# Kernel optimization log

Measured on AMD Instinct MI355X. Metric: run time of the kernel, lower is better.

Reference implementation:

```python
import jax, jax.numpy as jnp
import numpy as np

B, NA, NR, D, H, DH = 2, 4096, 512, 128, 8, 16
N_LOCAL, N_IPA, N_ITER = 5, 4, 3


def rots_from_vec(v):
    # quaternion (1, vx, vy, vz) normalized -> rotation matrix (AlphaFold-style update)
    q = jnp.concatenate([jnp.ones(v.shape[:-1] + (1,), v.dtype), v], axis=-1)
    q = q / jnp.linalg.norm(q, axis=-1, keepdims=True)
    w, x, y, z = q[..., 0], q[..., 1], q[..., 2], q[..., 3]
    R = jnp.stack([
        1 - 2 * (y * y + z * z), 2 * (x * y - w * z), 2 * (x * z + w * y),
        2 * (x * y + w * z), 1 - 2 * (x * x + z * z), 2 * (y * z - w * x),
        2 * (x * z - w * y), 2 * (y * z + w * x), 1 - 2 * (x * x + y * y)], axis=-1)
    return R.reshape(v.shape[:-1] + (3, 3))


def apply_frames(R, t, x):
    return jnp.einsum('...ij,...j->...i', R, x) + t


def invert_frames(R, t):
    Rt = jnp.swapaxes(R, -1, -2)
    return Rt, -jnp.einsum('...ij,...j->...i', Rt, t)


def pool_atoms_to_res(atom_feats, res_map):
    # scatter-mean: atoms -> residues
    d = atom_feats.shape[-1]
    idx = (res_map + jnp.arange(B, dtype=res_map.dtype)[:, None] * NR).reshape(-1)
    sums = jax.ops.segment_sum(atom_feats.reshape(-1, d), idx, num_segments=B * NR)
    cnts = jax.ops.segment_sum(jnp.ones((B * NA, 1), atom_feats.dtype), idx, num_segments=B * NR)
    return (sums / (cnts + 1e-8)).reshape(B, NR, d)


def setup_inputs() -> dict:
    key = jax.random.key(0)
    ks = iter(jax.random.split(key, 40))
    s = 0.02
    inp = dict(
        coords_bad=jax.random.normal(next(ks), (B, NA, 3), jnp.float32) * 5.0,
        atom_types=jax.random.randint(next(ks), (B, NA), 0, 20),
        residue_types=jax.random.randint(next(ks), (B, NA), 0, 21),
        mask=jnp.ones((B, NA), jnp.float32),
        res_mask=jnp.ones((B, NR), jnp.float32),
        res_map=jnp.sort(jax.random.randint(next(ks), (B, NA), 0, NR), axis=-1),
        rots_bad=rots_from_vec(0.1 * jax.random.normal(next(ks), (B, NR, 3), jnp.float32)),
        trans_bad=jax.random.normal(next(ks), (B, NR, 3), jnp.float32) * 5.0,
        atom_emb=jax.random.normal(next(ks), (20, D), jnp.float32) * s,
        res_emb=jax.random.normal(next(ks), (21, D), jnp.float32) * s,
        coord_W=jax.random.normal(next(ks), (3, D), jnp.float32) * s,
        coord_b=jnp.zeros((D,), jnp.float32),
        local_W=jax.random.normal(next(ks), (N_LOCAL, D, D), jnp.float32) * s,
        local_b=jnp.zeros((N_LOCAL, D), jnp.float32),
        pair_W=jax.random.normal(next(ks), (4, D), jnp.float32) * s,
        pair_b=jnp.zeros((D,), jnp.float32),
        ipa_Wq=jax.random.normal(next(ks), (N_IPA, D, H * DH), jnp.float32) * s,
        ipa_Wk=jax.random.normal(next(ks), (N_IPA, D, H * DH), jnp.float32) * s,
        ipa_Wv=jax.random.normal(next(ks), (N_IPA, D, H * DH), jnp.float32) * s,
        ipa_Wb=jax.random.normal(next(ks), (N_IPA, D, H), jnp.float32) * s,
        ipa_Wo=jax.random.normal(next(ks), (N_IPA, H * DH, D), jnp.float32) * s,
        ipa_bo=jnp.zeros((N_IPA, D), jnp.float32),
        head_W=jax.random.normal(next(ks), (D, 6), jnp.float32) * s,
        head_b=jnp.zeros((6,), jnp.float32),
    )
    return inp


def reference(coords_bad, atom_types, residue_types, mask, res_mask, res_map,
              rots_bad, trans_bad, atom_emb, res_emb, coord_W, coord_b,
              local_W, local_b, pair_W, pair_b,
              ipa_Wq, ipa_Wk, ipa_Wv, ipa_Wb, ipa_Wo, ipa_bo, head_W, head_b):
    cur_R, cur_t = rots_bad, trans_bad
    mask_j = (res_mask > 0)[:, None, None, :]  # [B,1,1,NR]
    # encoder output is iteration-invariant (coords_bad fixed), hoist it
    atom_feats = atom_emb[atom_types] + res_emb[residue_types] + coords_bad @ coord_W + coord_b
    feats0 = pool_atoms_to_res(atom_feats, res_map)  # [B,NR,D]
    for _ in range(N_ITER):
        feats = feats0
        residual = feats
        for l in range(N_LOCAL):
            feats = jax.nn.gelu(feats @ local_W[l] + local_b[l]) + residual
            residual = feats
        rel = cur_t[:, :, None, :] - cur_t[:, None, :, :]          # [B,NR,NR,3]
        dist = jnp.linalg.norm(rel, axis=-1, keepdims=True)
        pairwise = jnp.concatenate([rel, dist], axis=-1) @ pair_W + pair_b  # [B,NR,NR,D]
        for l in range(N_IPA):
            q = (feats @ ipa_Wq[l]).reshape(B, NR, H, DH)
            k = (feats @ ipa_Wk[l]).reshape(B, NR, H, DH)
            v = (feats @ ipa_Wv[l]).reshape(B, NR, H, DH)
            bias = jnp.transpose(pairwise @ ipa_Wb[l], (0, 3, 1, 2))  # [B,H,NR,NR]
            logits = jnp.einsum('bihd,bjhd->bhij', q, k) / np.float32(np.sqrt(DH)) + bias
            logits = jnp.where(mask_j, logits, jnp.float32(-1e9))
            attn = jax.nn.softmax(logits, axis=-1)
            o = jnp.einsum('bhij,bjhd->bihd', attn, v).reshape(B, NR, H * DH)
            feats = (o @ ipa_Wo[l] + ipa_bo[l]) + residual
            residual = feats
        upd = feats @ head_W + head_b                      # [B,NR,6]
        rot_vec, trans_vec = upd[..., :3], upd[..., 3:]
        cur_R = jnp.einsum('...ij,...jk->...ik', rots_from_vec(rot_vec), cur_R)
        cur_t = cur_t + jnp.einsum('...ij,...j->...i', cur_R, trans_vec)
        cur_t = cur_t * res_mask[..., None]
    inv_R, inv_t = invert_frames(rots_bad, trans_bad)
    bidx = jnp.arange(B)[:, None]
    local = apply_frames(inv_R[bidx, res_map], inv_t[bidx, res_map], coords_bad)
    final = apply_frames(jnp.swapaxes(cur_R[bidx, res_map], -1, -2), cur_t[bidx, res_map], local)
    return cur_R, cur_t, final
```

## Files before the change

kernel.cpp:

```cpp
#include <hip/hip_runtime.h>
#include <math.h>

#define B_ 2
#define NA_ 4096
#define NR_ 512
#define D_ 128
#define H_ 8
#define DH_ 16
#define NLOCAL_ 5
#define NIPA_ 4
#define NITER_ 3

typedef _Float16 half2_t __attribute__((ext_vector_type(2)));
typedef _Float16 f16x4 __attribute__((ext_vector_type(4)));
typedef float f32x4 __attribute__((ext_vector_type(4)));

#if __has_builtin(__builtin_amdgcn_fdot2)
#define FDOT2(a, b, c) __builtin_amdgcn_fdot2((a), (b), (c), false)
#else
__device__ __forceinline__ float FDOT2(half2_t a, half2_t b, float c) {
  return c + (float)a.x * (float)b.x + (float)a.y * (float)b.y;
}
#endif

#define MFMA16(a, b, c) __builtin_amdgcn_mfma_f32_16x16x16f16((a), (b), (c), 0, 0, 0)

__device__ __forceinline__ unsigned int pack_h(float a, float b) {
  union { unsigned int u; half2_t h; } x;
  x.h = half2_t{(_Float16)a, (_Float16)b};
  return x.u;
}
__device__ __forceinline__ half2_t u2h(unsigned int u) {
  union { unsigned int u; half2_t h; } x;
  x.u = u;
  return x.h;
}
__device__ __forceinline__ f16x4 mk4(unsigned int a, unsigned int b) {
  union { uint2 u; f16x4 h; } x;
  x.u = make_uint2(a, b);
  return x.h;
}
__device__ __forceinline__ float gelu_tanh(float x) {
  float x3 = x * x * x;
  return 0.5f * x * (1.0f + tanhf(0.7978845608028654f * (x + 0.044715f * x3)));
}

__device__ __forceinline__ void store_vT(unsigned int* vw, int h, int u, int rr,
                                         float b0, float b1) {
  unsigned int pk = pack_h(b0, b1);
  unsigned short* vt16 = (unsigned short*)vw;
  vt16[((h * 16 + 2 * u) << 10) + rr] = (unsigned short)(pk & 0xffffu);
  vt16[((h * 16 + 2 * u + 1) << 10) + rr] = (unsigned short)(pk >> 16);
}

__global__ __launch_bounds__(256) void k_setup(
    const float* __restrict__ coords, const int* __restrict__ atype,
    const int* __restrict__ rtype, const int* __restrict__ res_map,
    const float* __restrict__ rots_bad, const float* __restrict__ trans_bad,
    const float* __restrict__ res_mask,
    const float* __restrict__ atom_emb, const float* __restrict__ res_emb,
    const float* __restrict__ coord_W, const float* __restrict__ coord_b,
    const float* __restrict__ local_W, const float* __restrict__ pair_W,
    const float* __restrict__ pair_b, const float* __restrict__ Wq,
    const float* __restrict__ Wk, const float* __restrict__ Wv, const float* __restrict__ Wb,
    const float* __restrict__ Wo, float* __restrict__ feats0, float* __restrict__ weff,
    float* __restrict__ beff, float* __restrict__ curR, float* __restrict__ curT0,
    float4* __restrict__ ts4g0, unsigned int* __restrict__ lwh,
    unsigned int* __restrict__ qkvh, unsigned int* __restrict__ woh) {
  int tid = threadIdx.x, bid = blockIdx.x;
  int gtid = (bid << 8) + tid;
  for (int t = gtid; t < 172032; t += 65536) {
    if (t < 40960) {
      int c = t & 127, kk = (t >> 7) & 63, l = t >> 13;
      const float* s = local_W + (size_t)l * 16384 + (2 * kk) * 128 + c;
      lwh[t] = pack_h(s[0], s[128]);
    } else if (t < 139264) {
      int t2 = t - 40960;
      int c = t2 & 127, kk = (t2 >> 7) & 63, lm = t2 >> 13;
      int l = lm / 3, m = lm % 3;
      const float* base = (m == 0) ? Wq : ((m == 1) ? Wk : Wv);
      const float* s = base + (size_t)l * 16384 + (2 * kk) * 128 + c;
      qkvh[t2] = pack_h(s[0], s[128]);
    } else {
      int t3 = t - 139264;
      int c = t3 & 127, kk = (t3 >> 7) & 63, l = t3 >> 13;
      const float* s = Wo + (size_t)l * 16384 + (2 * kk) * 128 + c;
      woh[t3] = pack_h(s[0], s[128]);
    }
  }
  if (gtid < 160) {
    int l = gtid / 40, rest = gtid % 40;
    int c = rest / 8, h = rest & 7;
    const float* row = (c < 4) ? (pair_W + c * D_) : pair_b;
    float acc = 0.f;
    for (int d = 0; d < D_; d++) acc += row[d] * Wb[l * D_ * H_ + d * H_ + h];
    if (c < 4) weff[l * 32 + c * 8 + h] = acc;
    else beff[l * 8 + h] = acc;
  }
  if (gtid < 9216) curR[gtid] = rots_bad[gtid];
  else if (gtid < 12288) curT0[gtid - 9216] = trans_bad[gtid - 9216];
  if (gtid < 1024)
    ts4g0[gtid] = make_float4(trans_bad[gtid * 3], trans_bad[gtid * 3 + 1],
                              trans_bad[gtid * 3 + 2], res_mask[gtid]);
  for (int rp = 0; rp < 2; rp++) {
    int row = (bid << 2) + (rp << 1) + (tid >> 7);
    int d = tid & 127;
    int b = row >> 9, rr = row & (NR_ - 1);
    const int* rm = res_map + b * NA_;
    int lo = 0, hi = NA_;
    while (lo < hi) { int mid = (lo + hi) >> 1; if (rm[mid] < rr) lo = mid + 1; else hi = mid; }
    int start = lo;
    hi = NA_;
    while (lo < hi) { int mid = (lo + hi) >> 1; if (rm[mid] < rr + 1) lo = mid + 1; else hi = mid; }
    int end = lo;
    float w0 = coord_W[d], w1 = coord_W[D_ + d], w2 = coord_W[2 * D_ + d], cb = coord_b[d];
    float s = 0.f;
    for (int a = start; a < end; a++) {
      int ga = b * NA_ + a;
      s += atom_emb[atype[ga] * D_ + d] + res_emb[rtype[ga] * D_ + d] +
           coords[ga * 3 + 0] * w0 + coords[ga * 3 + 1] * w1 + coords[ga * 3 + 2] * w2 + cb;
    }
    feats0[row * D_ + d] = s / ((float)(end - start) + 1e-8f);
  }
}

__global__ __launch_bounds__(256) void k_localA(
    const float* __restrict__ feats0, const unsigned int* __restrict__ lwh,
    const float* __restrict__ local_b, const unsigned int* __restrict__ qkvh,
    float* __restrict__ featsL, unsigned int* __restrict__ qbU,
    unsigned int* __restrict__ kw, unsigned int* __restrict__ vw) {
  __shared__ unsigned int xh[4][64];
  __shared__ float xsf[4][128];
  int tid = threadIdx.x;
  int w = tid >> 6, cp = tid & 63;
  int row0 = blockIdx.x << 2;
  int row = row0 + w;
  float2 x2 = *(const float2*)(feats0 + (size_t)row * D_ + 2 * cp);
  float y0 = x2.x, y1 = x2.y;
  xsf[w][2 * cp] = y0; xsf[w][2 * cp + 1] = y1;
  xh[w][cp] = pack_h(y0, y1);
  for (int l = 0; l < NLOCAL_; l++) {
    const unsigned int* W = lwh + l * 8192;
    float a0 = 0.f, a1 = 0.f;
#pragma unroll 8
    for (int kk = 0; kk < 64; kk++) {
      uint2 ww = *(const uint2*)(W + kk * 128 + 2 * cp);
      half2_t x = u2h(xh[w][kk]);
      a0 = FDOT2(x, u2h(ww.x), a0);
      a1 = FDOT2(x, u2h(ww.y), a1);
    }
    y0 = gelu_tanh(a0 + local_b[l * D_ + 2 * cp]) + xsf[w][2 * cp];
    y1 = gelu_tanh(a1 + local_b[l * D_ + 2 * cp + 1]) + xsf[w][2 * cp + 1];
    xsf[w][2 * cp] = y0; xsf[w][2 * cp + 1] = y1;
    xh[w][cp] = pack_h(y0, y1);
  }
  *(float2*)(featsL + (size_t)row * D_ + 2 * cp) = make_float2(y0, y1);
  __syncthreads();
  if (w < 3) {
    const unsigned int* Wm = qkvh + (size_t)w * 8192;
    float bacc[4][2] = {};
#pragma unroll 8
    for (int kk = 0; kk < 64; kk++) {
      uint2 ww = *(const uint2*)(Wm + kk * 128 + 2 * cp);
#pragma unroll
      for (int r = 0; r < 4; r++) {
        half2_t x = u2h(xh[r][kk]);
        bacc[r][0] = FDOT2(x, u2h(ww.x), bacc[r][0]);
        bacc[r][1] = FDOT2(x, u2h(ww.y), bacc[r][1]);
      }
    }
    int h = cp >> 3, u = cp & 7;
#pragma unroll
    for (int r = 0; r < 4; r++) {
      int rr = row0 + r;
      if (w == 0) qbU[rr * 64 + cp] = pack_h(bacc[r][0], bacc[r][1]);
      else if (w == 1) kw[((h << 10) + rr) * 8 + u] = pack_h(bacc[r][0], bacc[r][1]);
      else store_vT(vw, h, u, rr, bacc[r][0], bacc[r][1]);
    }
  }
}

__global__ __launch_bounds__(256) void k_attn(
    const unsigned int* __restrict__ qbU, const unsigned int* __restrict__ kr,
    const unsigned int* __restrict__ vtg, const float4* __restrict__ ts4g,
    const float* __restrict__ weff, const float* __restrict__ beff,
    float* __restrict__ ob, int l) {
  __shared__ float4 ts4[NR_];
  __shared__ float pre[NR_];
  __shared__ float osum[4][64][5];
  int tid = threadIdx.x, bid = blockIdx.x;
  int w = tid >> 6, lane = tid & 63;
  int qt = bid & 31, bh = bid >> 5;
  int b = bh >> 3, h = bh & 7;
  float c0 = weff[l * 32 + h], c1 = weff[l * 32 + 8 + h];
  float c2 = weff[l * 32 + 16 + h], c3 = weff[l * 32 + 24 + h];
  float be = beff[l * 8 + h];
  for (int idx = tid; idx < NR_; idx += 256) {
    float4 t4 = ts4g[(b << 9) + idx];
    ts4[idx] = t4;
    pre[idx] = be - (c0 * t4.x + c1 * t4.y + c2 * t4.z);
  }
  __syncthreads();
  int lrow = lane & 15, lgrp = lane >> 4;
  int qrow = (b << 9) + qt * 16 + lrow;
  const uint2 qp = *(const uint2*)(qbU + (size_t)qrow * 64 + h * 8 + lgrp * 2);
  f16x4 qf = mk4(qp.x, qp.y);
  float4 ti = ts4[qt * 16 + lrow];
  float cti = c0 * ti.x + c1 * ti.y + c2 * ti.z;
  const unsigned int* kbase = kr + ((size_t)((h << 10) + (b << 9))) * 8;
  const unsigned int* vbase = vtg + (((h * 16 + lrow) << 9) + (b << 8));
  f32x4 zero = {0.f, 0.f, 0.f, 0.f};
  f32x4 oacc = zero;
  float lsum = 0.f;
#pragma unroll
  for (int jj = 0; jj < 8; jj++) {
    int jt = w * 8 + jj;
    int jr = jt * 16 + lrow;
    uint2 kp = *(const uint2*)(kbase + jr * 8 + lgrp * 2);
    f16x4 kf = mk4(kp.x, kp.y);
    f32x4 s = MFMA16(kf, qf, zero);
    f16x4 pv;
#pragma unroll
    for (int r = 0; r < 4; r++) {
      int j = jt * 16 + lgrp * 4 + r;
      float4 tj = ts4[j];
      float rx = ti.x - tj.x, ry = ti.y - tj.y, rz = ti.z - tj.z;
      float dist = sqrtf(rx * rx + ry * ry + rz * rz);
      float L = s[r] * 0.25f + cti + pre[j] + c3 * dist;
      L = (tj.w > 0.f) ? L : -1e9f;
      float p = __expf(L);
      lsum += p;
      pv[r] = (_Float16)p;
    }
    uint2 vp2 = *(const uint2*)(vbase + jt * 8 + lgrp * 2);
    f16x4 vf = mk4(vp2.x, vp2.y);
    oacc = MFMA16(vf, pv, oacc);
  }
  lsum += __shfl_xor(lsum, 16, 64);
  lsum += __shfl_xor(lsum, 32, 64);
  float* o = osum[w][lane];
  o[0] = oacc[0]; o[1] = oacc[1]; o[2] = oacc[2]; o[3] = oacc[3]; o[4] = lsum;
  __syncthreads();
  if (w == 0) {
    float s0 = 0.f, s1 = 0.f, s2 = 0.f, s3 = 0.f, sl = 0.f;
#pragma unroll
    for (int r = 0; r < 4; r++) {
      const float* p = osum[r][lane];
      s0 += p[0]; s1 += p[1]; s2 += p[2]; s3 += p[3]; sl += p[4];
    }
    float inv = 1.f / sl;
    float4 o4 = make_float4(s0 * inv, s1 * inv, s2 * inv, s3 * inv);
    *(float4*)(ob + (size_t)qrow * D_ + h * DH_ + lgrp * 4) = o4;
  }
}

__global__ __launch_bounds__(256) void k_oproj(
    const float* __restrict__ ob, const unsigned int* __restrict__ woh,
    const float* __restrict__ bo, const unsigned int* __restrict__ qkvh,
    const float* __restrict__ featsIn, float* __restrict__ featsW,
    const float* __restrict__ featsL, unsigned int* __restrict__ qbU,
    unsigned int* __restrict__ kw, unsigned int* __restrict__ vw,
    const float* __restrict__ curT_r, float* __restrict__ curT_w,
    float4* __restrict__ ts4g_w, float* __restrict__ curR,
    const float* __restrict__ res_mask, const float* __restrict__ head_W,
    const float* __restrict__ head_b, int l, int lastLayer, int doQ0) {
  __shared__ float part[4][2][128];
  __shared__ float xsf[2][128];
  __shared__ unsigned int xh[2][64];
  int tid = threadIdx.x;
  int w = tid >> 6, cp = tid & 63;
  int row0 = blockIdx.x << 1;
  if (w < 2) {
    float2 o2 = *(const float2*)(ob + (size_t)(row0 + w) * D_ + 2 * cp);
    xh[w][cp] = pack_h(o2.x, o2.y);
  }
  __syncthreads();
  {
    const unsigned int* W = woh + (size_t)l * 8192 + (w * 16) * 128;
    float a[2][2] = {};
#pragma unroll
    for (int kk = 0; kk < 16; kk++) {
      uint2 ww = *(const uint2*)(W + kk * 128 + 2 * cp);
#pragma unroll
      for (int r = 0; r < 2; r++) {
        half2_t x = u2h(xh[r][w * 16 + kk]);
        a[r][0] = FDOT2(x, u2h(ww.x), a[r][0]);
        a[r][1] = FDOT2(x, u2h(ww.y), a[r][1]);
      }
    }
#pragma unroll
    for (int r = 0; r < 2; r++) {
      part[w][r][2 * cp] = a[r][0];
      part[w][r][2 * cp + 1] = a[r][1];
    }
  }
  __syncthreads();
  {
    int r = tid >> 7, c = tid & 127;
    float f = part[0][r][c] + part[1][r][c] + part[2][r][c] + part[3][r][c] +
              bo[l * D_ + c] + featsIn[(size_t)(row0 + r) * D_ + c];
    featsW[(size_t)(row0 + r) * D_ + c] = f;
    xsf[r][c] = f;
  }
  __syncthreads();
  if (w < 2) xh[w][cp] = pack_h(xsf[w][2 * cp], xsf[w][2 * cp + 1]);
  __syncthreads();
  if (!lastLayer) {
    if (w < 3) {
      const unsigned int* Wm = qkvh + (size_t)((l + 1) * 3 + w) * 8192;
      float bacc[2][2] = {};
#pragma unroll 8
      for (int kk = 0; kk < 64; kk++) {
        uint2 ww = *(const uint2*)(Wm + kk * 128 + 2 * cp);
#pragma unroll
        for (int r = 0; r < 2; r++) {
          half2_t x = u2h(xh[r][kk]);
          bacc[r][0] = FDOT2(x, u2h(ww.x), bacc[r][0]);
          bacc[r][1] = FDOT2(x, u2h(ww.y), bacc[r][1]);
        }
      }
      int h = cp >> 3, u = cp & 7;
#pragma unroll
      for (int r = 0; r < 2; r++) {
        int rr = row0 + r;
        if (w == 0) qbU[rr * 64 + cp] = pack_h(bacc[r][0], bacc[r][1]);
        else if (w == 1) kw[((h << 10) + rr) * 8 + u] = pack_h(bacc[r][0], bacc[r][1]);
        else store_vT(vw, h, u, rr, bacc[r][0], bacc[r][1]);
      }
    }
  } else {
    if (w < 2) {
      int row = row0 + w;
      float f0 = xsf[w][2 * cp], f1 = xsf[w][2 * cp + 1];
      float pc[6];
#pragma unroll
      for (int c = 0; c < 6; c++)
        pc[c] = f0 * head_W[(2 * cp) * 6 + c] + f1 * head_W[(2 * cp + 1) * 6 + c];
#pragma unroll
      for (int m = 1; m < 64; m <<= 1)
#pragma unroll
        for (int c = 0; c < 6; c++) pc[c] += __shfl_xor(pc[c], m, 64);
      if (cp == 0) {
        float u[6];
#pragma unroll
        for (int c = 0; c < 6; c++) u[c] = pc[c] + head_b[c];
        float vx = u[0], vy = u[1], vz = u[2];
        float inv = rsqrtf(1.f + vx * vx + vy * vy + vz * vz);
        float qw = inv, qx = vx * inv, qy = vy * inv, qz = vz * inv;
        float Rd[9];
        Rd[0] = 1.f - 2.f * (qy * qy + qz * qz); Rd[1] = 2.f * (qx * qy - qw * qz);
        Rd[2] = 2.f * (qx * qz + qw * qy); Rd[3] = 2.f * (qx * qy + qw * qz);
        Rd[4] = 1.f - 2.f * (qx * qx + qz * qz); Rd[5] = 2.f * (qy * qz - qw * qx);
        Rd[6] = 2.f * (qx * qz - qw * qy); Rd[7] = 2.f * (qy * qz + qw * qx);
        Rd[8] = 1.f - 2.f * (qx * qx + qy * qy);
        float Ro[9];
#pragma unroll
        for (int c = 0; c < 9; c++) Ro[c] = curR[row * 9 + c];
        float Rn[9];
#pragma unroll
        for (int i2 = 0; i2 < 3; i2++)
#pragma unroll
          for (int kk = 0; kk < 3; kk++)
            Rn[i2 * 3 + kk] = Rd[i2 * 3 + 0] * Ro[0 * 3 + kk] +
                              Rd[i2 * 3 + 1] * Ro[1 * 3 + kk] +
                              Rd[i2 * 3 + 2] * Ro[2 * 3 + kk];
        float tx = curT_r[row * 3 + 0], ty = curT_r[row * 3 + 1], tz = curT_r[row * 3 + 2];
        float ux = u[3], uy = u[4], uz = u[5];
        float m = res_mask[row];
#pragma unroll
        for (int c = 0; c < 9; c++) curR[row * 9 + c] = Rn[c];
        float ntx = (tx + Rn[0] * ux + Rn[1] * uy + Rn[2] * uz) * m;
        float nty = (ty + Rn[3] * ux + Rn[4] * uy + Rn[5] * uz) * m;
        float ntz = (tz + Rn[6] * ux + Rn[7] * uy + Rn[8] * uz) * m;
        curT_w[row * 3 + 0] = ntx;
        curT_w[row * 3 + 1] = nty;
        curT_w[row * 3 + 2] = ntz;
        ts4g_w[row] = make_float4(ntx, nty, ntz, m);
      }
    }
    if (doQ0) {
      if (w < 2) {
        float2 fl = *(const float2*)(featsL + (size_t)(row0 + w) * D_ + 2 * cp);
        xh[w][cp] = pack_h(fl.x, fl.y);
      }
      __syncthreads();
      if (w < 3) {
        const unsigned int* Wm = qkvh + (size_t)w * 8192;
        float bacc[2][2] = {};
#pragma unroll 8
        for (int kk = 0; kk < 64; kk++) {
          uint2 ww = *(const uint2*)(Wm + kk * 128 + 2 * cp);
#pragma unroll
          for (int r = 0; r < 2; r++) {
            half2_t x = u2h(xh[r][kk]);
            bacc[r][0] = FDOT2(x, u2h(ww.x), bacc[r][0]);
            bacc[r][1] = FDOT2(x, u2h(ww.y), bacc[r][1]);
          }
        }
        int h = cp >> 3, u = cp & 7;
#pragma unroll
        for (int r = 0; r < 2; r++) {
          int rr = row0 + r;
          if (w == 0) qbU[rr * 64 + cp] = pack_h(bacc[r][0], bacc[r][1]);
          else if (w == 1) kw[((h << 10) + rr) * 8 + u] = pack_h(bacc[r][0], bacc[r][1]);
          else store_vT(vw, h, u, rr, bacc[r][0], bacc[r][1]);
        }
      }
    }
  }
}

__global__ void k_final(const float* __restrict__ coords, const int* __restrict__ res_map,
                        const float* __restrict__ rots_bad, const float* __restrict__ trans_bad,
                        const float* __restrict__ curR, const float* __restrict__ curT,
                        float* __restrict__ out) {
  int a = blockIdx.x * blockDim.x + threadIdx.x;
  if (a < B_ * NR_) {
#pragma unroll
    for (int c = 0; c < 9; c++) out[a * 9 + c] = curR[a * 9 + c];
    out[B_ * NR_ * 9 + a * 3 + 0] = curT[a * 3 + 0];
    out[B_ * NR_ * 9 + a * 3 + 1] = curT[a * 3 + 1];
    out[B_ * NR_ * 9 + a * 3 + 2] = curT[a * 3 + 2];
  }
  if (a >= B_ * NA_) return;
  int b = a / NA_;
  int r = b * NR_ + res_map[a];
  float x0 = coords[a * 3 + 0], x1 = coords[a * 3 + 1], x2 = coords[a * 3 + 2];
  float R0[9], Rc[9];
#pragma unroll
  for (int c = 0; c < 9; c++) { R0[c] = rots_bad[r * 9 + c]; Rc[c] = curR[r * 9 + c]; }
  float t0x = trans_bad[r * 3 + 0], t0y = trans_bad[r * 3 + 1], t0z = trans_bad[r * 3 + 2];
  float dx = x0 - t0x, dy = x1 - t0y, dz = x2 - t0z;
  float lx = R0[0] * dx + R0[3] * dy + R0[6] * dz;
  float ly = R0[1] * dx + R0[4] * dy + R0[7] * dz;
  float lz = R0[2] * dx + R0[5] * dy + R0[8] * dz;
  float tcx = curT[r * 3 + 0], tcy = curT[r * 3 + 1], tcz = curT[r * 3 + 2];
  float fx = Rc[0] * lx + Rc[3] * ly + Rc[6] * lz + tcx;
  float fy = Rc[1] * lx + Rc[4] * ly + Rc[7] * lz + tcy;
  float fz = Rc[2] * lx + Rc[5] * ly + Rc[8] * lz + tcz;
  int off = B_ * NR_ * 12;
  out[off + a * 3 + 0] = fx;
  out[off + a * 3 + 1] = fy;
  out[off + a * 3 + 2] = fz;
}

extern "C" void kernel_launch(void* const* d_in, const int* in_sizes, int n_in,
                              void* d_out, int out_size, void* d_ws, size_t ws_size,
                              hipStream_t stream) {
  const float* coords    = (const float*)d_in[0];
  const int*   atype     = (const int*)d_in[1];
  const int*   rtype     = (const int*)d_in[2];
  const float* res_mask  = (const float*)d_in[4];
  const int*   res_map   = (const int*)d_in[5];
  const float* rots_bad  = (const float*)d_in[6];
  const float* trans_bad = (const float*)d_in[7];
  const float* atom_emb  = (const float*)d_in[8];
  const float* res_emb   = (const float*)d_in[9];
  const float* coord_W   = (const float*)d_in[10];
  const float* coord_b   = (const float*)d_in[11];
  const float* local_W   = (const float*)d_in[12];
  const float* local_b   = (const float*)d_in[13];
  const float* pair_W    = (const float*)d_in[14];
  const float* pair_b    = (const float*)d_in[15];
  const float* Wq        = (const float*)d_in[16];
  const float* Wk        = (const float*)d_in[17];
  const float* Wv        = (const float*)d_in[18];
  const float* Wb        = (const float*)d_in[19];
  const float* Wo        = (const float*)d_in[20];
  const float* bo        = (const float*)d_in[21];
  const float* head_W    = (const float*)d_in[22];
  const float* head_b    = (const float*)d_in[23];

  float* ws = (float*)d_ws;
  float* ob     = ws;  ws += 131072;
  float* feats0 = ob;
  float* featsL = ws;  ws += 131072;
  float* featsW = ws;  ws += 131072;
  float* weff   = ws;  ws += 128;
  float* beff   = ws;  ws += 32;
  float* curR   = ws;  ws += 9216;
  float* curT0  = ws;  ws += 3072;
  float* curT1  = ws;  ws += 3072;
  float4* ts4g0 = (float4*)ws;  ws += 4096;
  float4* ts4g1 = (float4*)ws;  ws += 4096;
  unsigned int* wu = (unsigned int*)ws;
  unsigned int* qbU = wu;  wu += 65536;
  unsigned int* kbA = wu;  wu += 65536;
  unsigned int* vtA = wu;  wu += 65536;
  unsigned int* kbB = wu;  wu += 65536;
  unsigned int* vtB = wu;  wu += 65536;
  unsigned int* lwh  = wu; wu += 40960;
  unsigned int* qkvh = wu; wu += 98304;
  unsigned int* woh  = wu; wu += 32768;
  float* out = (float*)d_out;

  k_setup<<<256, 256, 0, stream>>>(coords, atype, rtype, res_map, rots_bad, trans_bad,
                                   res_mask, atom_emb, res_emb, coord_W, coord_b, local_W,
                                   pair_W, pair_b, Wq, Wk, Wv, Wb, Wo, feats0, weff, beff,
                                   curR, curT0, ts4g0, lwh, qkvh, woh);
  k_localA<<<256, 256, 0, stream>>>(feats0, lwh, local_b, qkvh, featsL, qbU, kbA, vtA);

  for (int iter = 0; iter < NITER_; iter++) {
    float* Tr = (iter & 1) ? curT1 : curT0;
    float* Tw = (iter & 1) ? curT0 : curT1;
    float4* Gr = (iter & 1) ? ts4g1 : ts4g0;
    float4* Gw = (iter & 1) ? ts4g0 : ts4g1;
    for (int l = 0; l < NIPA_; l++) {
      unsigned int* krd = (l & 1) ? kbB : kbA;
      unsigned int* vrd = (l & 1) ? vtB : vtA;
      unsigned int* kwr = (l & 1) ? kbA : kbB;
      unsigned int* vwr = (l & 1) ? vtA : vtB;
      k_attn<<<512, 256, 0, stream>>>(qbU, krd, vrd, Gr, weff, beff, ob, l);
      k_oproj<<<512, 256, 0, stream>>>(ob, woh, bo, qkvh, (l == 0) ? featsL : featsW,
                                       featsW, featsL, qbU, kwr, vwr, Tr, Tw, Gw, curR,
                                       res_mask, head_W, head_b, l,
                                       (l == NIPA_ - 1) ? 1 : 0,
                                       (l == NIPA_ - 1 && iter < NITER_ - 1) ? 1 : 0);
    }
  }
  k_final<<<(B_ * NA_ + 255) / 256, 256, 0, stream>>>(coords, res_map, rots_bad, trans_bad,
                                                      curR, curT1, out);
}
```

Before: 216.6 us.

## Fuse final frame application into last output-projection kernel

Removes the separate final kernel and computes the output frames and per-atom coordinates inside the last oproj launch. Each block binary-searches the sorted res_map to find its residue's atom range, using the new rotation and translation kept in shared memory. It also merges the residual-add and half-packing steps to drop one barrier. This saves a kernel launch and a global round trip of curR and curT, but it relies on res_map being sorted and gives the last launch uneven per-block atom work.

```diff
diff --git a/kernel.cpp b/kernel.cpp
--- a/kernel.cpp
+++ b/kernel.cpp
@@ -263,10 +263,14 @@
     const float* __restrict__ curT_r, float* __restrict__ curT_w,
     float4* __restrict__ ts4g_w, float* __restrict__ curR,
     const float* __restrict__ res_mask, const float* __restrict__ head_W,
-    const float* __restrict__ head_b, int l, int lastLayer, int doQ0) {
+    const float* __restrict__ head_b,
+    const float* __restrict__ coords, const int* __restrict__ res_map,
+    const float* __restrict__ rots_bad, const float* __restrict__ trans_bad,
+    float* __restrict__ outp, int l, int lastLayer, int doQ0, int doFinal) {
   __shared__ float part[4][2][128];
   __shared__ float xsf[2][128];
   __shared__ unsigned int xh[2][64];
+  __shared__ float fr[2][12];
   int tid = threadIdx.x;
   int w = tid >> 6, cp = tid & 63;
   int row0 = blockIdx.x << 1;
@@ -295,15 +299,18 @@
     }
   }
   __syncthreads();
-  {
-    int r = tid >> 7, c = tid & 127;
-    float f = part[0][r][c] + part[1][r][c] + part[2][r][c] + part[3][r][c] +
-              bo[l * D_ + c] + featsIn[(size_t)(row0 + r) * D_ + c];
-    featsW[(size_t)(row0 + r) * D_ + c] = f;
-    xsf[r][c] = f;
-  }
-  __syncthreads();
-  if (w < 2) xh[w][cp] = pack_h(xsf[w][2 * cp], xsf[w][2 * cp + 1]);
+  if (tid < 128) {
+    int r = tid >> 6, cpp = tid & 63;
+    int c0i = 2 * cpp;
+    float f0 = part[0][r][c0i] + part[1][r][c0i] + part[2][r][c0i] + part[3][r][c0i] +
+               bo[l * D_ + c0i] + featsIn[(size_t)(row0 + r) * D_ + c0i];
+    float f1 = part[0][r][c0i + 1] + part[1][r][c0i + 1] + part[2][r][c0i + 1] +
+               part[3][r][c0i + 1] + bo[l * D_ + c0i + 1] +
+               featsIn[(size_t)(row0 + r) * D_ + c0i + 1];
+    *(float2*)(featsW + (size_t)(row0 + r) * D_ + c0i) = make_float2(f0, f1);
+    xsf[r][c0i] = f0; xsf[r][c0i + 1] = f1;
+    xh[r][cpp] = pack_h(f0, f1);
+  }
   __syncthreads();
   if (!lastLayer) {
     if (w < 3) {
@@ -367,15 +374,21 @@
         float tx = curT_r[row * 3 + 0], ty = curT_r[row * 3 + 1], tz = curT_r[row * 3 + 2];
         float ux = u[3], uy = u[4], uz = u[5];
         float m = res_mask[row];
-#pragma unroll
-        for (int c = 0; c < 9; c++) curR[row * 9 + c] = Rn[c];
         float ntx = (tx + Rn[0] * ux + Rn[1] * uy + Rn[2] * uz) * m;
         float nty = (ty + Rn[3] * ux + Rn[4] * uy + Rn[5] * uz) * m;
         float ntz = (tz + Rn[6] * ux + Rn[7] * uy + Rn[8] * uz) * m;
-        curT_w[row * 3 + 0] = ntx;
-        curT_w[row * 3 + 1] = nty;
-        curT_w[row * 3 + 2] = ntz;
-        ts4g_w[row] = make_float4(ntx, nty, ntz, m);
+        if (!doFinal) {
+#pragma unroll
+          for (int c = 0; c < 9; c++) curR[row * 9 + c] = Rn[c];
+          curT_w[row * 3 + 0] = ntx;
+          curT_w[row * 3 + 1] = nty;
+          curT_w[row * 3 + 2] = ntz;
+          ts4g_w[row] = make_float4(ntx, nty, ntz, m);
+        } else {
+#pragma unroll
+          for (int c = 0; c < 9; c++) fr[w][c] = Rn[c];
+          fr[w][9] = ntx; fr[w][10] = nty; fr[w][11] = ntz;
+        }
       }
     }
     if (doQ0) {
@@ -407,41 +420,48 @@
         }
       }
     }
-  }
-}
-
-__global__ void k_final(const float* __restrict__ coords, const int* __restrict__ res_map,
-                        const float* __restrict__ rots_bad, const float* __restrict__ trans_bad,
-                        const float* __restrict__ curR, const float* __restrict__ curT,
-                        float* __restrict__ out) {
-  int a = blockIdx.x * blockDim.x + threadIdx.x;
-  if (a < B_ * NR_) {
-#pragma unroll
-    for (int c = 0; c < 9; c++) out[a * 9 + c] = curR[a * 9 + c];
-    out[B_ * NR_ * 9 + a * 3 + 0] = curT[a * 3 + 0];
-    out[B_ * NR_ * 9 + a * 3 + 1] = curT[a * 3 + 1];
-    out[B_ * NR_ * 9 + a * 3 + 2] = curT[a * 3 + 2];
-  }
-  if (a >= B_ * NA_) return;
-  int b = a / NA_;
-  int r = b * NR_ + res_map[a];
-  float x0 = coords[a * 3 + 0], x1 = coords[a * 3 + 1], x2 = coords[a * 3 + 2];
-  float R0[9], Rc[9];
-#pragma unroll
-  for (int c = 0; c < 9; c++) { R0[c] = rots_bad[r * 9 + c]; Rc[c] = curR[r * 9 + c]; }
-  float t0x = trans_bad[r * 3 + 0], t0y = trans_bad[r * 3 + 1], t0z = trans_bad[r * 3 + 2];
-  float dx = x0 - t0x, dy = x1 - t0y, dz = x2 - t0z;
-  float lx = R0[0] * dx + R0[3] * dy + R0[6] * dz;
-  float ly = R0[1] * dx + R0[4] * dy + R0[7] * dz;
-  float lz = R0[2] * dx + R0[5] * dy + R0[8] * dz;
-  float tcx = curT[r * 3 + 0], tcy = curT[r * 3 + 1], tcz = curT[r * 3 + 2];
-  float fx = Rc[0] * lx + Rc[3] * ly + Rc[6] * lz + tcx;
-  float fy = Rc[1] * lx + Rc[4] * ly + Rc[7] * lz + tcy;
-  float fz = Rc[2] * lx + Rc[5] * ly + Rc[8] * lz + tcz;
-  int off = B_ * NR_ * 12;
-  out[off + a * 3 + 0] = fx;
-  out[off + a * 3 + 1] = fy;
-  out[off + a * 3 + 2] = fz;
+    if (doFinal) {
+      __syncthreads();
+      if (tid < 24) {
+        int r = tid / 12, c = tid % 12;
+        int row = row0 + r;
+        if (c < 9) outp[row * 9 + c] = fr[r][c];
+        else outp[B_ * NR_ * 9 + row * 3 + (c - 9)] = fr[r][c];
+      }
+      int r = tid >> 7;
+      int idx = tid & 127;
+      int row = row0 + r;
+      int b = row >> 9, rr = row & (NR_ - 1);
+      const int* rm = res_map + b * NA_;
+      int lo = 0, hi = NA_;
+      while (lo < hi) { int mid = (lo + hi) >> 1; if (rm[mid] < rr) lo = mid + 1; else hi = mid; }
+      int start = lo;
+      hi = NA_;
+      while (lo < hi) { int mid = (lo + hi) >> 1; if (rm[mid] < rr + 1) lo = mid + 1; else hi = mid; }
+      int end = lo;
+      float R0[9], Rc[9];
+#pragma unroll
+      for (int c = 0; c < 9; c++) { R0[c] = rots_bad[row * 9 + c]; Rc[c] = fr[r][c]; }
+      float t0x = trans_bad[row * 3 + 0], t0y = trans_bad[row * 3 + 1];
+      float t0z = trans_bad[row * 3 + 2];
+      float tcx = fr[r][9], tcy = fr[r][10], tcz = fr[r][11];
+      int off = B_ * NR_ * 12;
+      for (int a = start + idx; a < end; a += 128) {
+        int ga = b * NA_ + a;
+        float x0 = coords[ga * 3 + 0], x1 = coords[ga * 3 + 1], x2 = coords[ga * 3 + 2];
+        float dx = x0 - t0x, dy = x1 - t0y, dz = x2 - t0z;
+        float lx = R0[0] * dx + R0[3] * dy + R0[6] * dz;
+        float ly = R0[1] * dx + R0[4] * dy + R0[7] * dz;
+        float lz = R0[2] * dx + R0[5] * dy + R0[8] * dz;
+        float fx = Rc[0] * lx + Rc[3] * ly + Rc[6] * lz + tcx;
+        float fy = Rc[1] * lx + Rc[4] * ly + Rc[7] * lz + tcy;
+        float fz = Rc[2] * lx + Rc[5] * ly + Rc[8] * lz + tcz;
+        outp[off + ga * 3 + 0] = fx;
+        outp[off + ga * 3 + 1] = fy;
+        outp[off + ga * 3 + 2] = fz;
+      }
+    }
+  }
 }
 
 extern "C" void kernel_launch(void* const* d_in, const int* in_sizes, int n_in,
@@ -510,14 +530,14 @@
       unsigned int* vrd = (l & 1) ? vtB : vtA;
       unsigned int* kwr = (l & 1) ? kbA : kbB;
       unsigned int* vwr = (l & 1) ? vtA : vtB;
+      int lastLayer = (l == NIPA_ - 1) ? 1 : 0;
+      int doQ0 = (lastLayer && iter < NITER_ - 1) ? 1 : 0;
+      int doFinal = (lastLayer && iter == NITER_ - 1) ? 1 : 0;
       k_attn<<<512, 256, 0, stream>>>(qbU, krd, vrd, Gr, weff, beff, ob, l);
       k_oproj<<<512, 256, 0, stream>>>(ob, woh, bo, qkvh, (l == 0) ? featsL : featsW,
                                        featsW, featsL, qbU, kwr, vwr, Tr, Tw, Gw, curR,
-                                       res_mask, head_W, head_b, l,
-                                       (l == NIPA_ - 1) ? 1 : 0,
-                                       (l == NIPA_ - 1 && iter < NITER_ - 1) ? 1 : 0);
-    }
-  }
-  k_final<<<(B_ * NA_ + 255) / 256, 256, 0, stream>>>(coords, res_map, rots_bad, trans_bad,
-                                                      curR, curT1, out);
-}
+                                       res_mask, head_W, head_b, coords, res_map, rots_bad,
+                                       trans_bad, out, l, lastLayer, doQ0, doFinal);
+    }
+  }
+}
```

New measurement: 217.3 us. About the same (+0.3%).
